# Kernel optimization log

Measured on AMD Instinct MI355X. Metric: run time of the kernel, lower is better.

## Reference

```python
import jax, jax.numpy as jnp
import numpy as np

N_SRC, N_DST, N_EDGES = 60000, 50000, 600000
IN_DIM, OUT_DIM = 256, 128


def setup_inputs() -> dict:
    key = jax.random.key(0)
    k1, k2, k3, k4, k5, k6 = jax.random.split(key, 6)
    features = jax.random.normal(k1, (N_SRC, IN_DIM), dtype=jnp.float32)
    t = jax.random.uniform(k2, (N_SRC,), dtype=jnp.float32)
    edge_src = jax.random.randint(k3, (N_EDGES,), 0, N_SRC, dtype=jnp.int32)
    edge_dst = jax.random.randint(k4, (N_EDGES,), 0, N_DST, dtype=jnp.int32)
    # learned params: xavier_normal with relu gain for fc, default for temporal_fc
    gain = float(np.sqrt(2.0))
    std_fc = gain * np.sqrt(2.0 / (IN_DIM + OUT_DIM))
    W_fc = jax.random.normal(k5, (OUT_DIM, IN_DIM), dtype=jnp.float32) * std_fc
    W_t = jax.random.normal(k6, (1, OUT_DIM), dtype=jnp.float32) * (1.0 / np.sqrt(OUT_DIM))
    return {"features": features, "t": t, "edge_src": edge_src,
            "edge_dst": edge_dst, "n_dst": N_DST, "W_fc": W_fc, "W_t": W_t}


def reference(features, t, edge_src, edge_dst, n_dst, W_fc, W_t):
    # z = fc(h), no bias
    z = features @ W_fc.T                      # [n_src, out_dim]
    s = (z @ W_t.T)[:, 0]                      # temporal_fc(z) -> [n_src]
    # edge attention: e = -|t_src - t_dst| (non-differentiable in original)
    e = jax.lax.stop_gradient(-jnp.abs(t[edge_src] - t[edge_dst]))  # [E]
    # mailbox logits: exp(temporal_fc(z_src) * e / 500)
    y = jnp.exp(s[edge_src] * e / 500.0)       # [E]
    # segment softmax over incoming edges of each dst node
    m = jax.ops.segment_max(y, edge_dst, num_segments=n_dst)
    m = jnp.where(jnp.isfinite(m), m, 0.0)     # empty mailboxes
    ex = jnp.exp(y - m[edge_dst])
    denom = jax.ops.segment_sum(ex, edge_dst, num_segments=n_dst)
    alpha = ex / denom[edge_dst]               # [E]
    # weighted neighbor sum
    h = jax.ops.segment_sum(alpha[:, None] * z[edge_src], edge_dst, num_segments=n_dst)
    # residual
    return z[:n_dst] + h
```

## Files before the change

### kernel.cpp

```cpp
#include <hip/hip_runtime.h>
#include <cstdint>

#define NBINS 1024
#define EPB   4096
#define MAXE  1536

typedef __attribute__((ext_vector_type(8))) _Float16 half8;
typedef __attribute__((ext_vector_type(4))) float floatx4;

__global__ __launch_bounds__(512, 4) void gemm_hist(
    const float* __restrict__ A, const float* __restrict__ W,
    const float* __restrict__ Wt, const int* __restrict__ edst,
    _Float16* __restrict__ z16, float* __restrict__ s,
    int* __restrict__ gcount, int M, int E, int NBH)
{
    __shared__ __align__(16) unsigned char smem[65536];

    if ((int)blockIdx.x < NBH) {
        int* h = (int*)smem;
        for (int i = threadIdx.x; i < NBINS; i += 512) h[i] = 0;
        __syncthreads();
        int base = blockIdx.x * EPB + threadIdx.x * 8;
        if (base + 8 <= E) {
            int4 d0 = *(const int4*)(edst + base);
            int4 d1 = *(const int4*)(edst + base + 4);
            atomicAdd(&h[d0.x >> 6], 1); atomicAdd(&h[d0.y >> 6], 1);
            atomicAdd(&h[d0.z >> 6], 1); atomicAdd(&h[d0.w >> 6], 1);
            atomicAdd(&h[d1.x >> 6], 1); atomicAdd(&h[d1.y >> 6], 1);
            atomicAdd(&h[d1.z >> 6], 1); atomicAdd(&h[d1.w >> 6], 1);
        } else {
            for (int i = 0; i < 8; ++i)
                if (base + i < E) atomicAdd(&h[edst[base + i] >> 6], 1);
        }
        __syncthreads();
        for (int i = threadIdx.x; i < NBINS; i += 512)
            gcount[(size_t)blockIdx.x * NBINS + i] = h[i];
        return;
    }

    half8* Wlds = (half8*)smem;
    const int tile = blockIdx.x - NBH;
    const int tid  = threadIdx.x;
    const int lane = tid & 63;
    const int w    = tid >> 6;
    const int m    = lane & 15;
    const int q    = lane >> 4;

#pragma unroll
    for (int it = 0; it < 8; ++it) {
        int pair = w * 8 + it;
        int nt = pair & 7, ks = pair >> 3;
        const float* src = W + (size_t)(nt * 16 + m) * 256 + ks * 32 + q * 8;
        float4 w0 = *(const float4*)src;
        float4 w1 = *(const float4*)(src + 4);
        half8 h;
        h[0] = (_Float16)w0.x; h[1] = (_Float16)w0.y;
        h[2] = (_Float16)w0.z; h[3] = (_Float16)w0.w;
        h[4] = (_Float16)w1.x; h[5] = (_Float16)w1.y;
        h[6] = (_Float16)w1.z; h[7] = (_Float16)w1.w;
        Wlds[pair * 64 + lane] = h;
    }

    const int row_base = tile * 128 + w * 16;
    const int arow = min(row_base + m, M - 1);
    const float* ap = A + (size_t)arow * 256 + q * 8;

    float4 abuf[8];
#pragma unroll
    for (int i = 0; i < 4; ++i) {
        abuf[2 * i]     = *(const float4*)(ap + i * 32);
        abuf[2 * i + 1] = *(const float4*)(ap + i * 32 + 4);
    }

    floatx4 acc[8];
#pragma unroll
    for (int nt = 0; nt < 8; ++nt) acc[nt] = (floatx4){0.f, 0.f, 0.f, 0.f};

    __syncthreads();

#pragma unroll
    for (int ks = 0; ks < 8; ++ks) {
        float4 a0 = abuf[(ks & 3) * 2];
        float4 a1 = abuf[(ks & 3) * 2 + 1];
        half8 af;
        af[0] = (_Float16)a0.x; af[1] = (_Float16)a0.y;
        af[2] = (_Float16)a0.z; af[3] = (_Float16)a0.w;
        af[4] = (_Float16)a1.x; af[5] = (_Float16)a1.y;
        af[6] = (_Float16)a1.z; af[7] = (_Float16)a1.w;

        if (ks < 4) {
            abuf[(ks & 3) * 2]     = *(const float4*)(ap + (ks + 4) * 32);
            abuf[(ks & 3) * 2 + 1] = *(const float4*)(ap + (ks + 4) * 32 + 4);
        }

#pragma unroll
        for (int nt = 0; nt < 8; ++nt) {
            half8 bf = Wlds[(ks * 8 + nt) * 64 + lane];
            acc[nt] = __builtin_amdgcn_mfma_f32_16x16x32_f16(
                af, bf, acc[nt], 0, 0, 0);
        }
    }

    float wt[8];
#pragma unroll
    for (int nt = 0; nt < 8; ++nt) wt[nt] = Wt[nt * 16 + m];

    float sp[4] = {0.f, 0.f, 0.f, 0.f};
#pragma unroll
    for (int nt = 0; nt < 8; ++nt)
#pragma unroll
        for (int reg = 0; reg < 4; ++reg)
            sp[reg] += acc[nt][reg] * wt[nt];

#pragma unroll
    for (int reg = 0; reg < 4; ++reg) {
        int row = row_base + q * 4 + reg;
        if (row < M) {
#pragma unroll
            for (int nt = 0; nt < 8; ++nt)
                z16[(size_t)row * 128 + nt * 16 + m] = (_Float16)acc[nt][reg];
        }
    }
#pragma unroll
    for (int off = 1; off <= 8; off <<= 1)
#pragma unroll
        for (int reg = 0; reg < 4; ++reg)
            sp[reg] += __shfl_xor(sp[reg], off, 64);
    if (m == 0) {
#pragma unroll
        for (int reg = 0; reg < 4; ++reg) {
            int row = row_base + q * 4 + reg;
            if (row < M) s[row] = sp[reg];
        }
    }
}

__global__ __launch_bounds__(256) void part_scan(
    int* __restrict__ gcount, int* __restrict__ binTot, int NB)
{
    int b    = blockIdx.x * 4 + (threadIdx.x >> 6);
    int lane = threadIdx.x & 63;
    if (b >= NBINS) return;
    int chunks = (NB + 63) >> 6;
    int run = 0;
    for (int c = 0; c < chunks; ++c) {
        int blk = c * 64 + lane;
        int v = (blk < NB) ? gcount[(size_t)blk * NBINS + b] : 0;
        int incl = v;
#pragma unroll
        for (int off = 1; off < 64; off <<= 1) {
            int n = __shfl_up(incl, off, 64);
            if (lane >= off) incl += n;
        }
        if (blk < NB) gcount[(size_t)blk * NBINS + b] = run + incl - v;
        run += __shfl(incl, 63, 64);
    }
    if (lane == 0) binTot[b] = run;
}

__global__ __launch_bounds__(1024) void part_scanB(
    const int* __restrict__ binTot, int* __restrict__ binstart)
{
    __shared__ int sb[NBINS];
    int b = threadIdx.x;
    int v = binTot[b];
    sb[b] = v;
    __syncthreads();
    for (int off = 1; off < NBINS; off <<= 1) {
        int add = (b >= off) ? sb[b - off] : 0;
        __syncthreads();
        sb[b] += add;
        __syncthreads();
    }
    binstart[b] = sb[b] - v;
    if (b == NBINS - 1) binstart[NBINS] = sb[b];
}

__global__ __launch_bounds__(512) void part_scatter(
    const int* __restrict__ esrc, const int* __restrict__ edst,
    const float* __restrict__ t, const float* __restrict__ s,
    const int* __restrict__ gcount, const int* __restrict__ binstart,
    int2* __restrict__ part, int E)
{
    __shared__ int hloc[NBINS];
    __shared__ int hbase[NBINS];
    for (int i = threadIdx.x; i < NBINS; i += 512) hloc[i] = 0;
    __syncthreads();

    int base = blockIdx.x * EPB + threadIdx.x * 8;
    int si[8], di[8], rk[8];
    int nv = 0;
    if (base < E) {
        nv = E - base; if (nv > 8) nv = 8;
        if (nv == 8) {
            int4 s0 = *(const int4*)(esrc + base);
            int4 s1 = *(const int4*)(esrc + base + 4);
            int4 d0 = *(const int4*)(edst + base);
            int4 d1 = *(const int4*)(edst + base + 4);
            si[0]=s0.x; si[1]=s0.y; si[2]=s0.z; si[3]=s0.w;
            si[4]=s1.x; si[5]=s1.y; si[6]=s1.z; si[7]=s1.w;
            di[0]=d0.x; di[1]=d0.y; di[2]=d0.z; di[3]=d0.w;
            di[4]=d1.x; di[5]=d1.y; di[6]=d1.z; di[7]=d1.w;
        } else {
            for (int i = 0; i < 8; ++i) {
                int e = min(base + i, E - 1);
                si[i] = esrc[e]; di[i] = edst[e];
            }
        }
#pragma unroll
        for (int i = 0; i < 8; ++i)
            if (i < nv) rk[i] = atomicAdd(&hloc[di[i] >> 6], 1);
    }

    for (int i = threadIdx.x; i < NBINS; i += 512)
        hbase[i] = binstart[i] + gcount[(size_t)blockIdx.x * NBINS + i];
    __syncthreads();

#pragma unroll
    for (int i = 0; i < 8; ++i) {
        if (i < nv) {
            float ee = -fabsf(t[si[i]] - t[di[i]]);
            float exv = __expf(__expf(s[si[i]] * ee * (1.0f / 500.0f)));
            part[hbase[di[i] >> 6] + rk[i]] =
                make_int2((si[i] & 0xffff) | ((di[i] & 63) << 16),
                          __float_as_int(exv));
        }
    }
}

__global__ __launch_bounds__(256) void aggregate(
    const _Float16* __restrict__ z16, const int* __restrict__ binstart,
    const int2* __restrict__ part, float* __restrict__ out, int Nd)
{
    __shared__ int2 arr[MAXE];
    __shared__ int lcnt[64];
    __shared__ int loff[65];

    const int tid = threadIdx.x;
    const int b = blockIdx.x;
    const int s0 = binstart[b];
    int nE = binstart[b + 1] - s0;
    if (nE > MAXE) nE = MAXE;

    if (tid < 64) lcnt[tid] = 0;
    __syncthreads();

    int2 rec[6]; int rrk[6], rloc[6], nrec = 0;
    for (int i = tid; i < nE; i += 256) {
        int2 r = part[s0 + i];
        int loc = (r.x >> 16) & 63;
        rec[nrec] = r;
        rloc[nrec] = loc;
        rrk[nrec] = atomicAdd(&lcnt[loc], 1);
        ++nrec;
    }
    __syncthreads();
    if (tid < 64) {
        int v = lcnt[tid], x = v;
#pragma unroll
        for (int off = 1; off < 64; off <<= 1) {
            int n = __shfl_up(x, off, 64);
            if (tid >= off) x += n;
        }
        loff[tid + 1] = x;
        if (tid == 0) loff[0] = 0;
    }
    __syncthreads();
    for (int i = 0; i < nrec; ++i)
        arr[loff[rloc[i]] + rrk[i]] = rec[i];
    __syncthreads();

    const int lane = tid & 63;
    const int w = tid >> 6;
    const int g = lane >> 3;
    const int c = lane & 7;

    const int loc0 = w * 16 + g;
    const int loc1 = loc0 + 8;
    const int jb0 = loff[loc0], je0 = loff[loc0 + 1];
    const int jb1 = loff[loc1], je1 = loff[loc1 + 1];
    int j0 = jb0, j1 = jb1;

    float acc0[16], acc1[16];
#pragma unroll
    for (int i = 0; i < 16; ++i) { acc0[i] = 0.f; acc1[i] = 0.f; }
    float ds0 = 0.f, ds1 = 0.f;

    while (j0 < je0 || j1 < je1) {
        bool vA0 = j0 < je0,     vB0 = j0 + 1 < je0;
        bool vA1 = j1 < je1,     vB1 = j1 + 1 < je1;
        int2 rA0 = arr[vA0 ? j0     : 0];
        int2 rB0 = arr[vB0 ? j0 + 1 : 0];
        int2 rA1 = arr[vA1 ? j1     : 0];
        int2 rB1 = arr[vB1 ? j1 + 1 : 0];
        float xA0 = vA0 ? __int_as_float(rA0.y) : 0.f;
        float xB0 = vB0 ? __int_as_float(rB0.y) : 0.f;
        float xA1 = vA1 ? __int_as_float(rA1.y) : 0.f;
        float xB1 = vB1 ? __int_as_float(rB1.y) : 0.f;
        const half8* pA0 = (const half8*)(z16 + (size_t)(rA0.x & 0xffff) * 128 + c * 16);
        const half8* pB0 = (const half8*)(z16 + (size_t)(rB0.x & 0xffff) * 128 + c * 16);
        const half8* pA1 = (const half8*)(z16 + (size_t)(rA1.x & 0xffff) * 128 + c * 16);
        const half8* pB1 = (const half8*)(z16 + (size_t)(rB1.x & 0xffff) * 128 + c * 16);
        half8 a0lo = pA0[0], a0hi = pA0[1];
        half8 b0lo = pB0[0], b0hi = pB0[1];
        half8 a1lo = pA1[0], a1hi = pA1[1];
        half8 b1lo = pB1[0], b1hi = pB1[1];
        ds0 += xA0 + xB0;
        ds1 += xA1 + xB1;
#pragma unroll
        for (int i = 0; i < 8; ++i) {
            acc0[i]     = fmaf(xA0, (float)a0lo[i], acc0[i]);
            acc0[8 + i] = fmaf(xA0, (float)a0hi[i], acc0[8 + i]);
            acc0[i]     = fmaf(xB0, (float)b0lo[i], acc0[i]);
            acc0[8 + i] = fmaf(xB0, (float)b0hi[i], acc0[8 + i]);
            acc1[i]     = fmaf(xA1, (float)a1lo[i], acc1[i]);
            acc1[8 + i] = fmaf(xA1, (float)a1hi[i], acc1[8 + i]);
            acc1[i]     = fmaf(xB1, (float)b1lo[i], acc1[i]);
            acc1[8 + i] = fmaf(xB1, (float)b1hi[i], acc1[8 + i]);
        }
        j0 += 2; j1 += 2;
    }

#pragma unroll
    for (int half = 0; half < 2; ++half) {
        int d = b * 64 + (half ? loc1 : loc0);
        if (d >= Nd) continue;
        float ds = half ? ds1 : ds0;
        float* ac = half ? acc1 : acc0;
        bool has = half ? (je1 > jb1) : (je0 > jb0);
        float inv = has ? 1.0f / ds : 0.0f;
        const half8* zr = (const half8*)(z16 + (size_t)d * 128 + c * 16);
        half8 r0 = zr[0], r1 = zr[1];
        float* op = out + (size_t)d * 128 + c * 16;
        *(float4*)(op + 0)  = make_float4(fmaf(ac[0],  inv, (float)r0[0]),
                                          fmaf(ac[1],  inv, (float)r0[1]),
                                          fmaf(ac[2],  inv, (float)r0[2]),
                                          fmaf(ac[3],  inv, (float)r0[3]));
        *(float4*)(op + 4)  = make_float4(fmaf(ac[4],  inv, (float)r0[4]),
                                          fmaf(ac[5],  inv, (float)r0[5]),
                                          fmaf(ac[6],  inv, (float)r0[6]),
                                          fmaf(ac[7],  inv, (float)r0[7]));
        *(float4*)(op + 8)  = make_float4(fmaf(ac[8],  inv, (float)r1[0]),
                                          fmaf(ac[9],  inv, (float)r1[1]),
                                          fmaf(ac[10], inv, (float)r1[2]),
                                          fmaf(ac[11], inv, (float)r1[3]));
        *(float4*)(op + 12) = make_float4(fmaf(ac[12], inv, (float)r1[4]),
                                          fmaf(ac[13], inv, (float)r1[5]),
                                          fmaf(ac[14], inv, (float)r1[6]),
                                          fmaf(ac[15], inv, (float)r1[7]));
    }
}

extern "C" void kernel_launch(void* const* d_in, const int* in_sizes, int n_in,
                              void* d_out, int out_size, void* d_ws, size_t ws_size,
                              hipStream_t stream)
{
    const float* features = (const float*)d_in[0];
    const float* t        = (const float*)d_in[1];
    const int*   esrc     = (const int*)d_in[2];
    const int*   edst     = (const int*)d_in[3];
    const float* Wfc      = (const float*)d_in[5];
    const float* Wt       = (const float*)d_in[6];
    float* out = (float*)d_out;

    const int M  = in_sizes[1];
    const int E  = in_sizes[2];
    const int OD = in_sizes[6];
    const int Nd = out_size / OD;

    const int NBH = (E + EPB - 1) / EPB;
    const int GB  = (M + 127) / 128;

    _Float16* z16      = (_Float16*)d_ws;
    float*    s        = (float*)(z16 + (size_t)M * 128);
    int*      gcount   = (int*)(s + M);
    int*      binTot   = gcount + (size_t)NBH * NBINS;
    int*      binstart = binTot + NBINS;
    int2*     part     = (int2*)(binstart + NBINS + 4);

    gemm_hist<<<NBH + GB, 512, 0, stream>>>(features, Wfc, Wt, edst,
                                            z16, s, gcount, M, E, NBH);
    part_scan<<<NBINS / 4, 256, 0, stream>>>(gcount, binTot, NBH);
    part_scanB<<<1, 1024, 0, stream>>>(binTot, binstart);
    part_scatter<<<NBH, 512, 0, stream>>>(esrc, edst, t, s, gcount, binstart,
                                          part, E);
    aggregate<<<(Nd + 63) / 64, 256, 0, stream>>>(z16, binstart, part, out, Nd);
}
```

Measured before the change: 177.0 us.

## Rework scans as serial-per-bin and wave-shuffle; give each aggregate thread group one dst node

part_scan now gives each bin its own thread and walks the blocks serially in coalesced rows, replacing the per-wave shuffle scan. part_scanB swaps the log-step shared-memory scan, which synchronises every step, for a two-level wave-shuffle scan. aggregate moves to 512 threads per block so each 8-lane group handles one destination node instead of two, with the edge loop unrolled by four for more gathers in flight. The trade is less work per thread and more waves for latency hiding against higher per-block register pressure under launch_bounds(512,4), and part_scan now has only 1024 threads.

```diff
diff --git a/kernel.cpp b/kernel.cpp
--- a/kernel.cpp
+++ b/kernel.cpp
@@ -138,42 +138,54 @@
 __global__ __launch_bounds__(256) void part_scan(
     int* __restrict__ gcount, int* __restrict__ binTot, int NB)
 {
-    int b    = blockIdx.x * 4 + (threadIdx.x >> 6);
-    int lane = threadIdx.x & 63;
-    if (b >= NBINS) return;
-    int chunks = (NB + 63) >> 6;
+    int b = blockIdx.x * 256 + threadIdx.x;
     int run = 0;
-    for (int c = 0; c < chunks; ++c) {
-        int blk = c * 64 + lane;
-        int v = (blk < NB) ? gcount[(size_t)blk * NBINS + b] : 0;
-        int incl = v;
-#pragma unroll
-        for (int off = 1; off < 64; off <<= 1) {
-            int n = __shfl_up(incl, off, 64);
-            if (lane >= off) incl += n;
-        }
-        if (blk < NB) gcount[(size_t)blk * NBINS + b] = run + incl - v;
-        run += __shfl(incl, 63, 64);
-    }
-    if (lane == 0) binTot[b] = run;
+    int blk = 0;
+    for (; blk + 4 <= NB; blk += 4) {
+        int v0 = gcount[(size_t)(blk + 0) * NBINS + b];
+        int v1 = gcount[(size_t)(blk + 1) * NBINS + b];
+        int v2 = gcount[(size_t)(blk + 2) * NBINS + b];
+        int v3 = gcount[(size_t)(blk + 3) * NBINS + b];
+        gcount[(size_t)(blk + 0) * NBINS + b] = run; run += v0;
+        gcount[(size_t)(blk + 1) * NBINS + b] = run; run += v1;
+        gcount[(size_t)(blk + 2) * NBINS + b] = run; run += v2;
+        gcount[(size_t)(blk + 3) * NBINS + b] = run; run += v3;
+    }
+    for (; blk < NB; ++blk) {
+        int v = gcount[(size_t)blk * NBINS + b];
+        gcount[(size_t)blk * NBINS + b] = run; run += v;
+    }
+    binTot[b] = run;
 }
 
 __global__ __launch_bounds__(1024) void part_scanB(
     const int* __restrict__ binTot, int* __restrict__ binstart)
 {
-    __shared__ int sb[NBINS];
+    __shared__ int wsum[16];
     int b = threadIdx.x;
+    int lane = b & 63, wv = b >> 6;
     int v = binTot[b];
-    sb[b] = v;
-    __syncthreads();
-    for (int off = 1; off < NBINS; off <<= 1) {
-        int add = (b >= off) ? sb[b - off] : 0;
-        __syncthreads();
-        sb[b] += add;
-        __syncthreads();
-    }
-    binstart[b] = sb[b] - v;
-    if (b == NBINS - 1) binstart[NBINS] = sb[b];
+    int x = v;
+#pragma unroll
+    for (int off = 1; off < 64; off <<= 1) {
+        int n = __shfl_up(x, off, 64);
+        if (lane >= off) x += n;
+    }
+    if (lane == 63) wsum[wv] = x;
+    __syncthreads();
+    if (b < 64) {
+        int t = (b < 16) ? wsum[b] : 0;
+#pragma unroll
+        for (int off = 1; off < 16; off <<= 1) {
+            int n = __shfl_up(t, off, 64);
+            if (lane >= off) t += n;
+        }
+        if (b < 16) wsum[b] = t;
+    }
+    __syncthreads();
+    int base = (wv > 0) ? wsum[wv - 1] : 0;
+    binstart[b] = base + x - v;
+    if (b == NBINS - 1) binstart[NBINS] = base + x;
 }
 
 __global__ __launch_bounds__(512) void part_scatter(
@@ -228,7 +240,7 @@
     }
 }
 
-__global__ __launch_bounds__(256) void aggregate(
+__global__ __launch_bounds__(512, 4) void aggregate(
     const _Float16* __restrict__ z16, const int* __restrict__ binstart,
     const int2* __restrict__ part, float* __restrict__ out, int Nd)
 {
@@ -245,8 +257,8 @@
     if (tid < 64) lcnt[tid] = 0;
     __syncthreads();
 
-    int2 rec[6]; int rrk[6], rloc[6], nrec = 0;
-    for (int i = tid; i < nE; i += 256) {
+    int2 rec[3]; int rrk[3], rloc[3], nrec = 0;
+    for (int i = tid; i < nE; i += 512) {
         int2 r = part[s0 + i];
         int loc = (r.x >> 16) & 63;
         rec[nrec] = r;
@@ -275,79 +287,69 @@
     const int g = lane >> 3;
     const int c = lane & 7;
 
-    const int loc0 = w * 16 + g;
-    const int loc1 = loc0 + 8;
-    const int jb0 = loff[loc0], je0 = loff[loc0 + 1];
-    const int jb1 = loff[loc1], je1 = loff[loc1 + 1];
-    int j0 = jb0, j1 = jb1;
-
-    float acc0[16], acc1[16];
-#pragma unroll
-    for (int i = 0; i < 16; ++i) { acc0[i] = 0.f; acc1[i] = 0.f; }
-    float ds0 = 0.f, ds1 = 0.f;
-
-    while (j0 < je0 || j1 < je1) {
-        bool vA0 = j0 < je0,     vB0 = j0 + 1 < je0;
-        bool vA1 = j1 < je1,     vB1 = j1 + 1 < je1;
-        int2 rA0 = arr[vA0 ? j0     : 0];
-        int2 rB0 = arr[vB0 ? j0 + 1 : 0];
-        int2 rA1 = arr[vA1 ? j1     : 0];
-        int2 rB1 = arr[vB1 ? j1 + 1 : 0];
-        float xA0 = vA0 ? __int_as_float(rA0.y) : 0.f;
-        float xB0 = vB0 ? __int_as_float(rB0.y) : 0.f;
-        float xA1 = vA1 ? __int_as_float(rA1.y) : 0.f;
-        float xB1 = vB1 ? __int_as_float(rB1.y) : 0.f;
-        const half8* pA0 = (const half8*)(z16 + (size_t)(rA0.x & 0xffff) * 128 + c * 16);
-        const half8* pB0 = (const half8*)(z16 + (size_t)(rB0.x & 0xffff) * 128 + c * 16);
-        const half8* pA1 = (const half8*)(z16 + (size_t)(rA1.x & 0xffff) * 128 + c * 16);
-        const half8* pB1 = (const half8*)(z16 + (size_t)(rB1.x & 0xffff) * 128 + c * 16);
-        half8 a0lo = pA0[0], a0hi = pA0[1];
-        half8 b0lo = pB0[0], b0hi = pB0[1];
-        half8 a1lo = pA1[0], a1hi = pA1[1];
-        half8 b1lo = pB1[0], b1hi = pB1[1];
-        ds0 += xA0 + xB0;
-        ds1 += xA1 + xB1;
+    const int loc = w * 8 + g;
+    const int jb = loff[loc], je = loff[loc + 1];
+
+    float acc[16];
+#pragma unroll
+    for (int i = 0; i < 16; ++i) acc[i] = 0.f;
+    float ds = 0.f;
+
+    for (int j = jb; j < je; j += 4) {
+        bool vB = j + 1 < je, vC = j + 2 < je, vD = j + 3 < je;
+        int2 rA = arr[j];
+        int2 rB = arr[vB ? j + 1 : 0];
+        int2 rC = arr[vC ? j + 2 : 0];
+        int2 rD = arr[vD ? j + 3 : 0];
+        float xA = __int_as_float(rA.y);
+        float xB = vB ? __int_as_float(rB.y) : 0.f;
+        float xC = vC ? __int_as_float(rC.y) : 0.f;
+        float xD = vD ? __int_as_float(rD.y) : 0.f;
+        const half8* pA = (const half8*)(z16 + (size_t)(rA.x & 0xffff) * 128 + c * 16);
+        const half8* pB = (const half8*)(z16 + (size_t)(rB.x & 0xffff) * 128 + c * 16);
+        const half8* pC = (const half8*)(z16 + (size_t)(rC.x & 0xffff) * 128 + c * 16);
+        const half8* pD = (const half8*)(z16 + (size_t)(rD.x & 0xffff) * 128 + c * 16);
+        half8 alo = pA[0], ahi = pA[1];
+        half8 blo = pB[0], bhi = pB[1];
+        half8 clo = pC[0], chi = pC[1];
+        half8 dlo = pD[0], dhi = pD[1];
+        ds += (xA + xB) + (xC + xD);
 #pragma unroll
         for (int i = 0; i < 8; ++i) {
-            acc0[i]     = fmaf(xA0, (float)a0lo[i], acc0[i]);
-            acc0[8 + i] = fmaf(xA0, (float)a0hi[i], acc0[8 + i]);
-            acc0[i]     = fmaf(xB0, (float)b0lo[i], acc0[i]);
-            acc0[8 + i] = fmaf(xB0, (float)b0hi[i], acc0[8 + i]);
-            acc1[i]     = fmaf(xA1, (float)a1lo[i], acc1[i]);
-            acc1[8 + i] = fmaf(xA1, (float)a1hi[i], acc1[8 + i]);
-            acc1[i]     = fmaf(xB1, (float)b1lo[i], acc1[i]);
-            acc1[8 + i] = fmaf(xB1, (float)b1hi[i], acc1[8 + i]);
-        }
-        j0 += 2; j1 += 2;
-    }
-
-#pragma unroll
-    for (int half = 0; half < 2; ++half) {
-        int d = b * 64 + (half ? loc1 : loc0);
-        if (d >= Nd) continue;
-        float ds = half ? ds1 : ds0;
-        float* ac = half ? acc1 : acc0;
-        bool has = half ? (je1 > jb1) : (je0 > jb0);
+            acc[i]     = fmaf(xA, (float)alo[i], acc[i]);
+            acc[8 + i] = fmaf(xA, (float)ahi[i], acc[8 + i]);
+            acc[i]     = fmaf(xB, (float)blo[i], acc[i]);
+            acc[8 + i] = fmaf(xB, (float)bhi[i], acc[8 + i]);
+            acc[i]     = fmaf(xC, (float)clo[i], acc[i]);
+            acc[8 + i] = fmaf(xC, (float)chi[i], acc[8 + i]);
+            acc[i]     = fmaf(xD, (float)dlo[i], acc[i]);
+            acc[8 + i] = fmaf(xD, (float)dhi[i], acc[8 + i]);
+        }
+    }
+
+    int d = b * 64 + loc;
+    if (d < Nd) {
+        bool has = je > jb;
         float inv = has ? 1.0f / ds : 0.0f;
         const half8* zr = (const half8*)(z16 + (size_t)d * 128 + c * 16);
         half8 r0 = zr[0], r1 = zr[1];
         float* op = out + (size_t)d * 128 + c * 16;
-        *(float4*)(op + 0)  = make_float4(fmaf(ac[0],  inv, (float)r0[0]),
-                                          fmaf(ac[1],  inv, (float)r0[1]),
-                                          fmaf(ac[2],  inv, (float)r0[2]),
-                                          fmaf(ac[3],  inv, (float)r0[3]));
-        *(float4*)(op + 4)  = make_float4(fmaf(ac[4],  inv, (float)r0[4]),
-                                          fmaf(ac[5],  inv, (float)r0[5]),
-                                          fmaf(ac[6],  inv, (float)r0[6]),
-                                          fmaf(ac[7],  inv, (float)r0[7]));
-        *(float4*)(op + 8)  = make_float4(fmaf(ac[8],  inv, (float)r1[0]),
-                                          fmaf(ac[9],  inv, (float)r1[1]),
-                                          fmaf(ac[10], inv, (float)r1[2]),
-                                          fmaf(ac[11], inv, (float)r1[3]));
-        *(float4*)(op + 12) = make_float4(fmaf(ac[12], inv, (float)r1[4]),
-                                          fmaf(ac[13], inv, (float)r1[5]),
-                                          fmaf(ac[14], inv, (float)r1[6]),
-                                          fmaf(ac[15], inv, (float)r1[7]));
+        *(float4*)(op + 0)  = make_float4(fmaf(acc[0],  inv, (float)r0[0]),
+                                          fmaf(acc[1],  inv, (float)r0[1]),
+                                          fmaf(acc[2],  inv, (float)r0[2]),
+                                          fmaf(acc[3],  inv, (float)r0[3]));
+        *(float4*)(op + 4)  = make_float4(fmaf(acc[4],  inv, (float)r0[4]),
+                                          fmaf(acc[5],  inv, (float)r0[5]),
+                                          fmaf(acc[6],  inv, (float)r0[6]),
+                                          fmaf(acc[7],  inv, (float)r0[7]));
+        *(float4*)(op + 8)  = make_float4(fmaf(acc[8],  inv, (float)r1[0]),
+                                          fmaf(acc[9],  inv, (float)r1[1]),
+                                          fmaf(acc[10], inv, (float)r1[2]),
+                                          fmaf(acc[11], inv, (float)r1[3]));
+        *(float4*)(op + 12) = make_float4(fmaf(acc[12], inv, (float)r1[4]),
+                                          fmaf(acc[13], inv, (float)r1[5]),
+                                          fmaf(acc[14], inv, (float)r1[6]),
+                                          fmaf(acc[15], inv, (float)r1[7]));
     }
 }
 
@@ -380,9 +382,9 @@
 
     gemm_hist<<<NBH + GB, 512, 0, stream>>>(features, Wfc, Wt, edst,
                                             z16, s, gcount, M, E, NBH);
-    part_scan<<<NBINS / 4, 256, 0, stream>>>(gcount, binTot, NBH);
+    part_scan<<<NBINS / 256, 256, 0, stream>>>(gcount, binTot, NBH);
     part_scanB<<<1, 1024, 0, stream>>>(binTot, binstart);
     part_scatter<<<NBH, 512, 0, stream>>>(esrc, edst, t, s, gcount, binstart,
                                           part, E);
-    aggregate<<<(Nd + 63) / 64, 256, 0, stream>>>(z16, binstart, part, out, Nd);
-}
+    aggregate<<<(Nd + 63) / 64, 512, 0, stream>>>(z16, binstart, part, out, Nd);
+}
```

Result: slower. 199.4 us (+12.6%).
